# Performance work log

Measured on AMD Instinct MI355X. Metric: run time of the kernel, lower is better.

Reference implementation:

```python
import jax, jax.numpy as jnp
import numpy as np

N_WIRES = 14
N_LAYERS = 3
DIM = 2 ** N_WIRES
BATCH = 1024


def _rx(theta):
    # RX(t) = [[cos t/2, -i sin t/2], [-i sin t/2, cos t/2]]
    c = jnp.cos(theta / 2).astype(jnp.complex64)
    s = jnp.sin(theta / 2).astype(jnp.complex64)
    return jnp.stack([jnp.stack([c, -1j * s]), jnp.stack([-1j * s, c])])


def _ry(theta):
    # RY(t) = [[cos t/2, -sin t/2], [sin t/2, cos t/2]]
    c = jnp.cos(theta / 2).astype(jnp.complex64)
    s = jnp.sin(theta / 2).astype(jnp.complex64)
    return jnp.stack([jnp.stack([c, -s]), jnp.stack([s, c])])


def _apply_1q(psi, U, w):
    # psi: (B, 2, 2, ..., 2); apply 2x2 U on qubit axis w+1
    psi = jnp.tensordot(psi, U, axes=((w + 1,), (1,)))  # contracted axis moves to end
    return jnp.moveaxis(psi, -1, w + 1)


def _apply_cnot(psi, c, t):
    # control qubit c, target qubit t (Python ints)
    a0 = jax.lax.index_in_dim(psi, 0, axis=c + 1, keepdims=True)
    a1 = jax.lax.index_in_dim(psi, 1, axis=c + 1, keepdims=True)
    a1 = jnp.flip(a1, axis=t + 1)  # X on target within control=1 subspace
    return jnp.concatenate([a0, a1], axis=c + 1)


def _circuit_features(state, params):
    # state: (B, 2**n) real normalized amplitudes -> PauliZ expvals (B, n)
    n = N_WIRES
    psi = state.astype(jnp.complex64).reshape((-1,) + (2,) * n)
    for layer in range(N_LAYERS):
        for w in range(n):
            psi = _apply_1q(psi, _rx(params[layer, w, 0]), w)
            psi = _apply_1q(psi, _ry(params[layer, w, 1]), w)
        for w in range(n - 1):
            psi = _apply_cnot(psi, w, w + 1)
        psi = _apply_cnot(psi, n - 1, 0)
    probs = jnp.real(psi * jnp.conj(psi))  # (B, 2, ..., 2)
    feats = []
    for w in range(n):
        axes = tuple(a for a in range(1, n + 1) if a != w + 1)
        p = jnp.sum(probs, axis=axes)  # (B, 2)
        feats.append(p[:, 0] - p[:, 1])  # <Z_w>
    return jnp.stack(feats, axis=1)  # (B, n)


def setup_inputs() -> dict:
    key = jax.random.key(0)
    k1, k2, k3 = jax.random.split(key, 3)
    state = jax.random.normal(k1, (BATCH, DIM), dtype=jnp.float32)
    state = state / jnp.linalg.norm(state, axis=1, keepdims=True)  # valid statevectors
    params = jax.random.normal(k2, (N_LAYERS, N_WIRES, 2), dtype=jnp.float32)
    head_w = jax.random.normal(k3, (1, N_WIRES), dtype=jnp.float32) * (1.0 / np.sqrt(N_WIRES))
    head_b = jnp.zeros((1,), dtype=jnp.float32)
    return {"state": state, "params": params, "head_w": head_w, "head_b": head_b}


def reference(state, params, head_w, head_b):
    feats = _circuit_features(state, params)          # (B, n_wires)
    out = feats @ head_w.T + head_b                   # (B, 1)
    return out[:, 0]                                  # (B,)
```

## Files before the change

kernel.cpp:

```cpp
#include <hip/hip_runtime.h>
#include <utility>

#define NW 14
#define NL 3
#define DIM 16384
#define NG  (NL * NW)
#define TPB 1024
#define NPH3 11

typedef float v2f __attribute__((ext_vector_type(2)));

struct S3 {
    int ok = 1;
    unsigned Lane[NPH3][6] = {};
    unsigned Reg[NPH3][4]  = {};
    unsigned Vw[4]         = {};
    unsigned WT[NPH3][6]   = {};
    unsigned WS[NPH3][16]  = {};
    unsigned pv[NPH3][4]   = {};
    unsigned cp[NPH3][4]   = {};
    unsigned ST[10] = {}, STK[4] = {}, STJ[4] = {};
    unsigned pz[NW] = {}, nib[NW] = {};
};

struct Bas14 { unsigned piv[14] = {}; int n = 0; };
constexpr bool binsert(Bas14& B, unsigned v) {
    unsigned x = v;
    for (int bit = 13; bit >= 0; --bit) {
        if (!((x >> bit) & 1u)) continue;
        if (B.piv[bit]) x ^= B.piv[bit];
        else { B.piv[bit] = x; ++B.n; return true; }
    }
    return false;
}

struct Ech { unsigned pv14[14] = {}; unsigned pc14[14] = {}; int ok = 1; };
constexpr Ech mkech(const unsigned bas[14]) {
    Ech E{};
    for (int b = 0; b < 14; ++b) {
        unsigned x = bas[b], c = 1u << b;
        for (int bit = 13; bit >= 0; --bit) {
            if (!((x >> bit) & 1u)) continue;
            if (E.pv14[bit]) { x ^= E.pv14[bit]; c ^= E.pc14[bit]; }
            else { E.pv14[bit] = x; E.pc14[bit] = c; x = 0; break; }
        }
        if (x) E.ok = 0;
    }
    return E;
}
constexpr unsigned coordsE(const Ech& E, unsigned v, int& ok) {
    unsigned x = v, c = 0;
    for (int bit = 13; bit >= 0; --bit) {
        if ((x >> bit) & 1u) {
            if (!E.pv14[bit]) { ok = 0; return 0; }
            x ^= E.pv14[bit]; c ^= E.pc14[bit];
        }
    }
    return c;
}

constexpr S3 build3(int vskip) {
    S3 S{};
    unsigned mk[NG] = {}, vmg[NG] = {}, zm[NW] = {};
    {
        unsigned A[NW] = {};
        for (int w = 0; w < NW; ++w) A[w] = 1u << (NW - 1 - w);
        int g = 0;
        for (int l = 0; l < NL; ++l) {
            unsigned rows[NW] = {};
            for (int u = 0; u < NW; ++u) rows[u] = A[u] | (1u << (NW + u));
            for (int col = 0; col < NW; ++col) {
                int piv = col;
                while (piv < NW && !((rows[piv] >> col) & 1u)) ++piv;
                if (piv >= NW) { S.ok = 0; continue; }
                unsigned tmp = rows[col]; rows[col] = rows[piv]; rows[piv] = tmp;
                for (int r = 0; r < NW; ++r)
                    if (r != col && ((rows[r] >> col) & 1u)) rows[r] ^= rows[col];
            }
            for (int w = 0; w < NW; ++w) {
                unsigned m = 0;
                for (int r = 0; r < NW; ++r) m |= ((rows[r] >> (NW + w)) & 1u) << r;
                mk[g] = m; vmg[g] = A[w]; ++g;
            }
            for (int w = 0; w < NW - 1; ++w) A[w + 1] ^= A[w];
            A[0] ^= A[NW - 1];
        }
        for (int w = 0; w < NW; ++w) zm[w] = A[w];
    }
    for (int p = 0; p < NPH3; ++p) {
        int J = (p < 10) ? 4 : 2;
        for (int q = 0; q < J; ++q) S.Reg[p][q] = mk[4 * p + q];
    }
    {
        Bas14 gb[6] = {};
        for (int g = 0; g < 6; ++g) {
            int nm = (g < 5) ? 8 : 2;
            for (int i = 0; i < nm; ++i) binsert(gb[g], mk[8 * g + i]);
        }
        int found = 0, skipped = 0;
        for (unsigned seed = 1; seed < 512u && !found; ++seed) {
            unsigned cand[4] = {};
            for (int i = 0; i < 4; ++i) {
                unsigned h = (seed * 2654435761u) ^ ((unsigned)(i + 1) * 0x9E3779B9u);
                h ^= h >> 15; h *= 2246822519u; h ^= h >> 13; h *= 3266489917u; h ^= h >> 16;
                cand[i] = h & 0x3FFFu;
            }
            Bas14 cb{};
            bool good = binsert(cb, cand[0]) && binsert(cb, cand[1])
                     && binsert(cb, cand[2]) && binsert(cb, cand[3]);
            for (int g = 0; g < 6 && good; ++g) {
                Bas14 t = gb[g];
                for (int i = 0; i < 4 && good; ++i)
                    if (!binsert(t, cand[i])) good = false;
            }
            if (good) {
                if (skipped < vskip) { ++skipped; continue; }
                for (int i = 0; i < 4; ++i) S.Vw[i] = cand[i];
                found = 1;
            }
        }
        if (!found) S.ok = 0;
    }
    for (int g = 0; g < 6; ++g) {
        int nm = (g < 5) ? 8 : 2;
        Bas14 B{};
        for (int i = 0; i < 4; ++i) binsert(B, S.Vw[i]);
        for (int i = 0; i < nm; ++i) binsert(B, mk[8 * g + i]);
        unsigned fill[12] = {}; int nf = 0;
        for (int b = 0; b < 14 && B.n < 14; ++b)
            if (binsert(B, 1u << b)) fill[nf++] = 1u << b;
        if (B.n != 14) S.ok = 0;
        if (g < 5) {
            int pA = 2 * g, pB = 2 * g + 1;
            for (int b = 0; b < 4; ++b) { S.Lane[pA][b] = S.Reg[pB][b]; S.Lane[pB][b] = S.Reg[pA][b]; }
            S.Lane[pA][4] = fill[0]; S.Lane[pA][5] = fill[1];
            S.Lane[pB][4] = fill[0]; S.Lane[pB][5] = fill[1];
        } else {
            S.Reg[10][2] = fill[0]; S.Reg[10][3] = fill[1];
            for (int b = 0; b < 6; ++b) S.Lane[10][b] = fill[2 + b];
        }
    }
    for (int t = NPH3 - 2; t >= 0; --t) {
        unsigned bas[14] = {};
        for (int b = 0; b < 6; ++b) bas[b] = S.Lane[t + 1][b];
        for (int q = 0; q < 4; ++q) bas[6 + q] = S.Reg[t + 1][q];
        for (int j = 0; j < 4; ++j) bas[10 + j] = S.Vw[j];
        Ech E = mkech(bas);
        if (!E.ok) S.ok = 0;
        unsigned rb[4] = {}; int rn = 0;
        for (int b = 0; b < 6; ++b) {
            int bestcs = 0, bestg = -1; unsigned bestr = 0;
            for (int cs = 0; cs < 16; ++cs) {
                unsigned c = 0;
                for (int q = 0; q < 4; ++q) if ((cs >> q) & 1) c ^= S.Reg[t][q];
                int ok2 = 1;
                unsigned r = coordsE(E, S.Lane[t][b] ^ c, ok2) & 15u;
                if (!ok2) continue;
                unsigned x = r;
                for (int i = 0; i < rn; ++i) {
                    int hb = 3; while (hb > 0 && !((rb[i] >> hb) & 1u)) --hb;
                    if ((x >> hb) & 1u) x ^= rb[i];
                }
                int gain = x ? 1 : 0;
                if (gain > bestg) { bestg = gain; bestcs = cs; bestr = r; }
                if (gain == 1) break;
            }
            unsigned c = 0;
            for (int q = 0; q < 4; ++q) if ((bestcs >> q) & 1) c ^= S.Reg[t][q];
            S.Lane[t][b] ^= c;
            unsigned x = bestr;
            for (int i = 0; i < rn; ++i) {
                int hb = 3; while (hb > 0 && !((rb[i] >> hb) & 1u)) --hb;
                if ((x >> hb) & 1u) x ^= rb[i];
            }
            if (x && rn < 4) rb[rn++] = x;
        }
        int okc = 1;
        for (int b = 0; b < 6; ++b) S.WT[t][b] = coordsE(E, S.Lane[t][b], okc);
        for (int s = 0; s < 16; ++s) {
            unsigned v = 0;
            for (int q = 0; q < 4; ++q) if ((s >> q) & 1) v ^= S.Reg[t][q];
            S.WS[t][s] = coordsE(E, v, okc);
        }
        if (!okc) S.ok = 0;
        for (int ub = 0; ub < 10; ++ub) {
            unsigned wamp = (ub < 6) ? S.Lane[t][ub] : S.Vw[ub - 6];
            unsigned widx = (ub < 6) ? S.WT[t][ub] : (1u << (10 + ub - 6));
            unsigned ramp = 0;
            for (int b = 0; b < 6; ++b) if ((widx >> b) & 1u) ramp ^= S.Lane[t + 1][b];
            for (int q = 0; q < 4; ++q) if ((widx >> (6 + q)) & 1u) ramp ^= S.Reg[t + 1][q];
            for (int j = 0; j < 4; ++j) if ((widx >> (10 + j)) & 1u) ramp ^= S.Vw[j];
            if (ramp != wamp) S.ok = 0;
        }
        for (int q = 0; q < 4; ++q) {
            unsigned widx = S.WS[t][1u << q];
            unsigned ramp = 0;
            for (int b = 0; b < 6; ++b) if ((widx >> b) & 1u) ramp ^= S.Lane[t + 1][b];
            for (int qq = 0; qq < 4; ++qq) if ((widx >> (6 + qq)) & 1u) ramp ^= S.Reg[t + 1][qq];
            for (int j = 0; j < 4; ++j) if ((widx >> (10 + j)) & 1u) ramp ^= S.Vw[j];
            if (ramp != S.Reg[t][q]) S.ok = 0;
        }
    }
    for (int p = 0; p < NPH3; ++p) {
        int J = (p < 10) ? 4 : 2;
        for (int q = 0; q < J; ++q) {
            unsigned vm = vmg[4 * p + q], pvm = 0;
            for (int b = 0; b < 6; ++b)
                if (__builtin_popcount(S.Lane[p][b] & vm) & 1) pvm |= 1u << b;
            for (int j = 0; j < 4; ++j)
                if (__builtin_popcount(S.Vw[j] & vm) & 1) pvm |= 1u << (6 + j);
            S.pv[p][q] = pvm;
            unsigned cpm = 0;
            for (int s = 0; s < 16; ++s) {
                unsigned v = 0;
                for (int q2 = 0; q2 < 4; ++q2) if ((s >> q2) & 1) v ^= S.Reg[p][q2];
                if (__builtin_popcount(v & vm) & 1) cpm |= 1u << s;
            }
            S.cp[p][q] = cpm;
        }
    }
    {
        unsigned bas[14] = {};
        for (int b = 0; b < 6; ++b) bas[b] = S.Lane[0][b];
        for (int q = 0; q < 4; ++q) bas[6 + q] = S.Reg[0][q];
        for (int j = 0; j < 4; ++j) bas[10 + j] = S.Vw[j];
        Ech E = mkech(bas);
        if (!E.ok) S.ok = 0;
        int okc = 1;
        for (int b = 0; b < 10; ++b) S.ST[b] = coordsE(E, 1u << (b + 2), okc);
        for (int k = 0; k < 4; ++k) S.STK[k] = coordsE(E, (unsigned)k << 12, okc);
        for (int j = 0; j < 4; ++j) S.STJ[j] = coordsE(E, (unsigned)j, okc);
        if (!okc) S.ok = 0;
        for (int ub = 0; ub < 18; ++ub) {
            unsigned amp = (ub < 10) ? (1u << (ub + 2))
                         : (ub < 14) ? ((unsigned)(ub - 10) << 12) : (unsigned)(ub - 14);
            unsigned widx = (ub < 10) ? S.ST[ub] : (ub < 14) ? S.STK[ub - 10] : S.STJ[ub - 14];
            unsigned ramp = 0;
            for (int b = 0; b < 6; ++b) if ((widx >> b) & 1u) ramp ^= S.Lane[0][b];
            for (int q = 0; q < 4; ++q) if ((widx >> (6 + q)) & 1u) ramp ^= S.Reg[0][q];
            for (int j = 0; j < 4; ++j) if ((widx >> (10 + j)) & 1u) ramp ^= S.Vw[j];
            if (ramp != amp) S.ok = 0;
        }
    }
    for (int w = 0; w < NW; ++w) {
        unsigned pzm = 0;
        for (int b = 0; b < 6; ++b)
            if (__builtin_popcount(S.Lane[10][b] & zm[w]) & 1) pzm |= 1u << b;
        for (int j = 0; j < 4; ++j)
            if (__builtin_popcount(S.Vw[j] & zm[w]) & 1) pzm |= 1u << (6 + j);
        S.pz[w] = pzm;
        unsigned nv = 0;
        for (int q = 0; q < 4; ++q)
            if (__builtin_popcount(S.Reg[10][q] & zm[w]) & 1) nv |= 1u << q;
        S.nib[w] = nv;
    }
    return S;
}
constexpr S3 pickBuild() {
    for (int v = 0; v < 4; ++v) {
        S3 s = build3(v);
        if (s.ok) return s;
    }
    S3 bad{}; bad.ok = 0; return bad;
}
constexpr S3 SC3 = pickBuild();
static_assert(SC3.ok == 1, "schedule build failed");

template<class F, unsigned... I>
__device__ __forceinline__ void static_for_impl(F&& f, std::integer_sequence<unsigned, I...>) {
    (f(std::integral_constant<unsigned, I>{}), ...);
}
template<unsigned N, class F>
__device__ __forceinline__ void static_for(F&& f) {
    static_for_impl(static_cast<F&&>(f), std::make_integer_sequence<unsigned, N>{});
}

template<int NEGLO, int NEGHI>
__device__ __forceinline__ v2f cmul(v2f k, v2f x) {
    v2f y;
    if constexpr (!NEGLO)
        asm("v_pk_mul_f32 %0, %1, %2 op_sel:[0,0] op_sel_hi:[0,1]"
            : "=&v"(y) : "v"(k), "v"(x));
    else
        asm("v_pk_mul_f32 %0, %1, %2 op_sel:[0,0] op_sel_hi:[0,1] neg_lo:[1,0] neg_hi:[1,0]"
            : "=&v"(y) : "v"(k), "v"(x));
    if constexpr (!NEGHI)
        asm("v_pk_fma_f32 %0, %1, %2, %0 op_sel:[1,1,0] op_sel_hi:[1,0,1] neg_lo:[0,1,0]"
            : "+v"(y) : "v"(k), "v"(x));
    else
        asm("v_pk_fma_f32 %0, %1, %2, %0 op_sel:[1,1,0] op_sel_hi:[1,0,1] neg_lo:[1,1,0] neg_hi:[1,0,0]"
            : "+v"(y) : "v"(k), "v"(x));
    return y;
}
template<int NEGLO, int NEGHI>
__device__ __forceinline__ void cmac(v2f& y, v2f k, v2f x) {
    if constexpr (!NEGLO)
        asm("v_pk_fma_f32 %0, %1, %2, %0 op_sel:[0,0,0] op_sel_hi:[0,1,1]"
            : "+v"(y) : "v"(k), "v"(x));
    else
        asm("v_pk_fma_f32 %0, %1, %2, %0 op_sel:[0,0,0] op_sel_hi:[0,1,1] neg_lo:[1,0,0] neg_hi:[1,0,0]"
            : "+v"(y) : "v"(k), "v"(x));
    if constexpr (!NEGHI)
        asm("v_pk_fma_f32 %0, %1, %2, %0 op_sel:[1,1,0] op_sel_hi:[1,0,1] neg_lo:[0,1,0]"
            : "+v"(y) : "v"(k), "v"(x));
    else
        asm("v_pk_fma_f32 %0, %1, %2, %0 op_sel:[1,1,0] op_sel_hi:[1,0,1] neg_lo:[1,1,0] neg_hi:[1,0,0]"
            : "+v"(y) : "v"(k), "v"(x));
}
template<bool CS> __device__ __forceinline__ v2f  cmulA(v2f k, v2f x) { return cmul<0, CS ? 1 : 0>(k, x); }
template<bool CS> __device__ __forceinline__ void cmacB(v2f& y, v2f k, v2f x) { cmac<CS ? 1 : 0, 0>(y, k, x); }

template<int P>
__device__ __forceinline__ void gates(v2f* x, const float4* __restrict__ umat, unsigned tid)
{
    static_for<4>([&](auto Qc) {
        constexpr int q = (int)decltype(Qc)::value;
        if constexpr (q < ((P < 10) ? 4 : 2)) {
            constexpr unsigned cp  = SC3.cp[P][q];
            constexpr unsigned pvm = SC3.pv[P][q];
            const float4 u = umat[4 * P + q];
            const unsigned sm = ((unsigned)__popc(tid & pvm)) << 31;
            v2f A, B;
            A.x = u.x; A.y = __uint_as_float(__float_as_uint(u.y) ^ sm);
            B.x = __uint_as_float(__float_as_uint(u.z) ^ sm); B.y = u.w;
            static_for<8>([&](auto Pp) {
                constexpr unsigned pp   = decltype(Pp)::value;
                constexpr unsigned lowm = (1u << q) - 1u;
                constexpr unsigned s0   = ((pp & ~lowm) << 1) | (pp & lowm);
                constexpr unsigned s1   = s0 | (1u << q);
                constexpr bool c0 = (cp >> s0) & 1u;
                constexpr bool c1 = (cp >> s1) & 1u;
                const v2f x0 = x[s0], x1 = x[s1];
                v2f y0 = cmulA<c0>(A, x0); cmacB<c0>(y0, B, x1);
                v2f y1 = cmulA<c1>(A, x1); cmacB<c1>(y1, B, x0);
                x[s0] = y0; x[s1] = y1;
            });
        }
    });
}

__device__ __forceinline__ void rdall(v2f* x, const char* psiB, unsigned rbase) {
    static_for<16>([&](auto Sc) {
        constexpr int s = (int)decltype(Sc)::value;
        x[s] = *(const v2f*)(psiB + rbase + (s << 9));
    });
}

template<int P>
__device__ __forceinline__ void wrt(char* psiB, unsigned tid, const v2f* x) {
    unsigned wi = ((tid >> 6) & 15u) << 10;
    static_for<6>([&](auto Bc) {
        constexpr int b = (int)decltype(Bc)::value;
        constexpr unsigned m = SC3.WT[P][b];
        wi ^= m & (unsigned)(-(int)((tid >> b) & 1u));
    });
    const unsigned wib = wi << 3;
    static_for<16>([&](auto Sc) {
        constexpr int s = (int)decltype(Sc)::value;
        constexpr unsigned off = SC3.WS[P][s] << 3;
        *(v2f*)(psiB + (wib ^ off)) = x[s];
    });
}

__device__ __forceinline__ void stageW(char* psiB, const float* __restrict__ gsrc,
                                       unsigned tid, unsigned sidx) {
    const float4* st4 = reinterpret_cast<const float4*>(gsrc);
    static_for<4>([&](auto Kc) {
        constexpr int k = (int)decltype(Kc)::value;
        float4 v = st4[tid + k * TPB];
        const unsigned bi = sidx ^ SC3.STK[k];
        *(v2f*)(psiB + ((bi ^ SC3.STJ[0]) << 3)) = (v2f){ v.x, 0.f };
        *(v2f*)(psiB + ((bi ^ SC3.STJ[1]) << 3)) = (v2f){ v.y, 0.f };
        *(v2f*)(psiB + ((bi ^ SC3.STJ[2]) << 3)) = (v2f){ v.z, 0.f };
        *(v2f*)(psiB + ((bi ^ SC3.STJ[3]) << 3)) = (v2f){ v.w, 0.f };
    });
}

__global__ __launch_bounds__(TPB, 4) void qsim_kernel(
    const float* __restrict__ state,
    const float* __restrict__ params,
    const float* __restrict__ head_w,
    const float* __restrict__ head_b,
    float* __restrict__ out)
{
    __shared__ v2f    psi[DIM];
    __shared__ float4 umat[NG];
    __shared__ float  red[2 * (TPB / 64)];
    char* psiB = (char*)psi;
    const unsigned tid = threadIdx.x;

    if (tid < NG) {
        float t1 = 0.5f * params[2 * tid + 0];
        float t2 = 0.5f * params[2 * tid + 1];
        float s1, c1, s2, c2;
        sincosf(t1, &s1, &c1);
        sincosf(t2, &s2, &c2);
        umat[tid] = make_float4(c1 * c2, s1 * s2, -s2 * c1, -c2 * s1);
    }

    const float* gA = state + (size_t)(2 * blockIdx.x) * DIM;
    const float* gB = gA + DIM;

    unsigned sidx = 0;
    static_for<10>([&](auto Bc) {
        constexpr int b = (int)decltype(Bc)::value;
        sidx ^= SC3.ST[b] & (unsigned)(-(int)((tid >> b) & 1u));
    });
    const unsigned rbase = ((tid >> 6) << 13) | ((tid & 63u) << 3);

    v2f xA[16], xB[16];

    stageW(psiB, gA, tid, sidx);
    __syncthreads();
    rdall(xA, psiB, rbase);
    __syncthreads();
    stageW(psiB, gB, tid, sidx);
    gates<0>(xA, umat, tid);
    __syncthreads();
    rdall(xB, psiB, rbase);
    __syncthreads();

    static_for<10>([&](auto Pc) {
        constexpr int P = (int)decltype(Pc)::value;
        wrt<P>(psiB, tid, xA);
        gates<P>(xB, umat, tid);
        __syncthreads();
        rdall(xA, psiB, rbase);
        __syncthreads();
        wrt<P>(psiB, tid, xB);
        gates<P + 1>(xA, umat, tid);
        __syncthreads();
        rdall(xB, psiB, rbase);
        __syncthreads();
    });
    gates<10>(xB, umat, tid);

    float e[NW];
    static_for<NW>([&](auto Wc) {
        constexpr int w = (int)decltype(Wc)::value;
        constexpr unsigned pzw = SC3.pz[w];
        float hw = head_w[w];
        e[w] = (__popc(tid & pzw) & 1) ? -hw : hw;
    });
    float c[16];
    static_for<16>([&](auto Mc) { c[decltype(Mc)::value] = 0.f; });
    static_for<NW>([&](auto Wc) {
        constexpr int w = (int)decltype(Wc)::value;
        c[SC3.nib[w]] += e[w];
    });
    static_for<4>([&](auto Bc) {
        constexpr unsigned B = 1u << decltype(Bc)::value;
        static_for<16>([&](auto Kc) {
            constexpr unsigned k = decltype(Kc)::value;
            if constexpr (!(k & B)) {
                float a = c[k], b = c[k | B];
                c[k] = a + b; c[k | B] = a - b;
            }
        });
    });
    float accA = 0.f, accB = 0.f;
    static_for<16>([&](auto Sc) {
        constexpr int s = (int)decltype(Sc)::value;
        accA += (xA[s].x * xA[s].x + xA[s].y * xA[s].y) * c[s];
        accB += (xB[s].x * xB[s].x + xB[s].y * xB[s].y) * c[s];
    });

#pragma unroll
    for (int off = 32; off > 0; off >>= 1) {
        accA += __shfl_down(accA, off, 64);
        accB += __shfl_down(accB, off, 64);
    }
    const unsigned lane = tid & 63, wv = tid >> 6;
    if (lane == 0) { red[wv] = accA; red[(TPB / 64) + wv] = accB; }
    __syncthreads();
    if (tid == 0) {
        float tA = 0.f, tB = 0.f;
#pragma unroll
        for (int i = 0; i < TPB / 64; ++i) { tA += red[i]; tB += red[(TPB / 64) + i]; }
        out[2 * blockIdx.x + 0] = tA + head_b[0];
        out[2 * blockIdx.x + 1] = tB + head_b[0];
    }
}

extern "C" void kernel_launch(void* const* d_in, const int* in_sizes, int n_in,
                              void* d_out, int out_size, void* d_ws, size_t ws_size,
                              hipStream_t stream) {
    const float* state  = (const float*)d_in[0];
    const float* params = (const float*)d_in[1];
    const float* head_w = (const float*)d_in[2];
    const float* head_b = (const float*)d_in[3];
    float* out = (float*)d_out;

    qsim_kernel<<<out_size / 2, TPB, 0, stream>>>(state, params, head_w, head_b, out);
}
```

Baseline: 128.7 us.

## Split gate phases across barriers and prefetch both state rows upfront

Each phase's four gate applications are split in half, so the second half runs after the LDS read and overlaps the barrier wait. Both batch rows' global loads are also issued at kernel start into registers instead of loading the second row later. This aims to hide barrier and global-memory latency by putting independent ALU work between synchronisations. The trade is higher register pressure (two extra float4[4] live sets) under a 4-blocks-per-SM launch bound, which could cause spills.

```diff
diff --git a/kernel.cpp b/kernel.cpp
--- a/kernel.cpp
+++ b/kernel.cpp
@@ -310,11 +310,11 @@
 template<bool CS> __device__ __forceinline__ v2f  cmulA(v2f k, v2f x) { return cmul<0, CS ? 1 : 0>(k, x); }
 template<bool CS> __device__ __forceinline__ void cmacB(v2f& y, v2f k, v2f x) { cmac<CS ? 1 : 0, 0>(y, k, x); }
 
-template<int P>
+template<int P, int Q0, int Q1>
 __device__ __forceinline__ void gates(v2f* x, const float4* __restrict__ umat, unsigned tid)
 {
-    static_for<4>([&](auto Qc) {
-        constexpr int q = (int)decltype(Qc)::value;
+    static_for<Q1 - Q0>([&](auto Qc) {
+        constexpr int q = Q0 + (int)decltype(Qc)::value;
         if constexpr (q < ((P < 10) ? 4 : 2)) {
             constexpr unsigned cp  = SC3.cp[P][q];
             constexpr unsigned pvm = SC3.pv[P][q];
@@ -362,17 +362,14 @@
     });
 }
 
-__device__ __forceinline__ void stageW(char* psiB, const float* __restrict__ gsrc,
-                                       unsigned tid, unsigned sidx) {
-    const float4* st4 = reinterpret_cast<const float4*>(gsrc);
+__device__ __forceinline__ void stageWreg(char* psiB, const float4* v, unsigned sidx) {
     static_for<4>([&](auto Kc) {
         constexpr int k = (int)decltype(Kc)::value;
-        float4 v = st4[tid + k * TPB];
         const unsigned bi = sidx ^ SC3.STK[k];
-        *(v2f*)(psiB + ((bi ^ SC3.STJ[0]) << 3)) = (v2f){ v.x, 0.f };
-        *(v2f*)(psiB + ((bi ^ SC3.STJ[1]) << 3)) = (v2f){ v.y, 0.f };
-        *(v2f*)(psiB + ((bi ^ SC3.STJ[2]) << 3)) = (v2f){ v.z, 0.f };
-        *(v2f*)(psiB + ((bi ^ SC3.STJ[3]) << 3)) = (v2f){ v.w, 0.f };
+        *(v2f*)(psiB + ((bi ^ SC3.STJ[0]) << 3)) = (v2f){ v[k].x, 0.f };
+        *(v2f*)(psiB + ((bi ^ SC3.STJ[1]) << 3)) = (v2f){ v[k].y, 0.f };
+        *(v2f*)(psiB + ((bi ^ SC3.STJ[2]) << 3)) = (v2f){ v[k].z, 0.f };
+        *(v2f*)(psiB + ((bi ^ SC3.STJ[3]) << 3)) = (v2f){ v[k].w, 0.f };
     });
 }
 
@@ -398,8 +395,8 @@
         umat[tid] = make_float4(c1 * c2, s1 * s2, -s2 * c1, -c2 * s1);
     }
 
-    const float* gA = state + (size_t)(2 * blockIdx.x) * DIM;
-    const float* gB = gA + DIM;
+    const float4* st4A = reinterpret_cast<const float4*>(state + (size_t)(2 * blockIdx.x) * DIM);
+    const float4* st4B = st4A + DIM / 4;
 
     unsigned sidx = 0;
     static_for<10>([&](auto Bc) {
@@ -410,12 +407,18 @@
 
     v2f xA[16], xB[16];
 
-    stageW(psiB, gA, tid, sidx);
+    float4 vA[4], vB[4];
+    static_for<4>([&](auto Kc) {
+        constexpr int k = (int)decltype(Kc)::value;
+        vA[k] = st4A[tid + k * TPB];
+        vB[k] = st4B[tid + k * TPB];
+    });
+    stageWreg(psiB, vA, sidx);
     __syncthreads();
     rdall(xA, psiB, rbase);
     __syncthreads();
-    stageW(psiB, gB, tid, sidx);
-    gates<0>(xA, umat, tid);
+    stageWreg(psiB, vB, sidx);
+    gates<0, 0, 4>(xA, umat, tid);
     __syncthreads();
     rdall(xB, psiB, rbase);
     __syncthreads();
@@ -423,17 +426,19 @@
     static_for<10>([&](auto Pc) {
         constexpr int P = (int)decltype(Pc)::value;
         wrt<P>(psiB, tid, xA);
-        gates<P>(xB, umat, tid);
+        gates<P, 0, 2>(xB, umat, tid);
         __syncthreads();
         rdall(xA, psiB, rbase);
+        gates<P, 2, 4>(xB, umat, tid);
         __syncthreads();
         wrt<P>(psiB, tid, xB);
-        gates<P + 1>(xA, umat, tid);
+        gates<P + 1, 0, 2>(xA, umat, tid);
         __syncthreads();
         rdall(xB, psiB, rbase);
+        gates<P + 1, 2, 4>(xA, umat, tid);
         __syncthreads();
     });
-    gates<10>(xB, umat, tid);
+    gates<10, 0, 4>(xB, umat, tid);
 
     float e[NW];
     static_for<NW>([&](auto Wc) {
```

After: 131.1 us. No clear change (+1.9%).
